# Kernel tuning notes

Hardware: AMD Instinct MI355X
Metric: run time of the kernel (lower is better)

## Reference

```python
import jax, jax.numpy as jnp
import numpy as np

N_EMBD = 384
HEAD_SIZE = 64
BLOCK_SIZE = 256

def setup_inputs() -> dict:
    key = jax.random.key(0)
    kx, kk, kq, kv = jax.random.split(key, 4)
    bound = 1.0 / np.sqrt(N_EMBD)  # torch nn.Linear default init
    return {
        "x": jax.random.normal(kx, (512, 256, N_EMBD), dtype=jnp.float32),
        "Wk": jax.random.uniform(kk, (N_EMBD, HEAD_SIZE), jnp.float32, -bound, bound),
        "Wq": jax.random.uniform(kq, (N_EMBD, HEAD_SIZE), jnp.float32, -bound, bound),
        "Wv": jax.random.uniform(kv, (N_EMBD, HEAD_SIZE), jnp.float32, -bound, bound),
    }

def reference(x, Wk, Wq, Wv):
    # x: [B, T, C]; single causal self-attention head (eval mode: dropout off)
    B, T, C = x.shape
    k = jnp.einsum('btc,ch->bth', x, Wk)   # [B, T, H]
    q = jnp.einsum('btc,ch->bth', x, Wq)
    v = jnp.einsum('btc,ch->bth', x, Wv)
    scale = 1.0 / jnp.sqrt(jnp.asarray(k.shape[-1], dtype=x.dtype))
    wei = jnp.einsum('bth,bsh->bts', q, k) * scale  # [B, T, T]
    causal = jnp.tril(jnp.ones((T, T), dtype=bool))
    wei = jnp.where(causal, wei, -jnp.inf)
    wei = jax.nn.softmax(wei, axis=-1)
    return jnp.einsum('bts,bsh->bth', wei, v)  # [B, T, H]
```

## Files before the change

kernel.cpp:

```cpp
#include <hip/hip_runtime.h>

#define T_DIM 256
#define C_DIM 384
#define H_DIM 64

typedef __attribute__((ext_vector_type(4))) float f32x4;
typedef __attribute__((ext_vector_type(8))) short bf16x8;
typedef unsigned short u16;

__device__ __forceinline__ u16 f2b(float f) {
  unsigned u = __float_as_uint(f);
  u = (u + 0x7FFFu + ((u >> 16) & 1u)) >> 16;
  return (u16)u;
}

__device__ __forceinline__ int sw64(int r, int c)  { return r * 64  + (c ^ ((r & 7) << 3)); }
__device__ __forceinline__ int sw256(int h, int t) { return h * 256 + (t ^ ((h & 7) << 3)); }
__device__ __forceinline__ int sw32(int r, int c)  { return r * 32  + (c ^ (((r >> 1) & 3) << 3)); }

__global__ __launch_bounds__(512, 2)
void head_fused(const float* __restrict__ x,
                const float* __restrict__ Wk,
                const float* __restrict__ Wq,
                const float* __restrict__ Wv,
                float* __restrict__ out)
{
  __shared__ u16 qs[T_DIM * H_DIM];
  __shared__ u16 ks[T_DIM * H_DIM];
  __shared__ u16 vT[H_DIM * T_DIM];
  __shared__ u16 un[16384];

  u16* xs  = un;
  u16* wsT = un + 8192;

  const int tid  = threadIdx.x;
  const int wv   = tid >> 6;
  const int lane = tid & 63;
  const int g    = lane >> 4;
  const int lr   = lane & 15;
  const int b    = blockIdx.x;

  const float* xb = x + (size_t)b * (T_DIM * C_DIM);

  int xr[4], xc[4];
#pragma unroll
  for (int it = 0; it < 4; ++it) {
    int idx = tid + it * 512;
    xr[it] = idx >> 3;
    xc[it] = (idx & 7) * 4;
  }
  int wrow[3], wcc[3];
  const float* wsrc[3];
#pragma unroll
  for (int it = 0; it < 3; ++it) {
    int idx = tid + it * 512;
    int q   = idx >> 5;
    int cc  = idx & 31;
    int seg = q >> 4;
    int hq  = q & 15;
    wrow[it] = seg * 64 + hq * 4;
    wcc[it]  = cc;
    wsrc[it] = ((seg == 0) ? Wq : (seg == 1) ? Wk : Wv) + hq * 4;
  }

  f32x4 acc[2][12];
#pragma unroll
  for (int mi = 0; mi < 2; ++mi)
#pragma unroll
    for (int nj = 0; nj < 12; ++nj)
      acc[mi][nj] = (f32x4){0.f, 0.f, 0.f, 0.f};

  f32x4 px[4], pwv[3];
#pragma unroll
  for (int it = 0; it < 4; ++it)
    px[it] = *reinterpret_cast<const f32x4*>(xb + xr[it] * C_DIM + xc[it]);
#pragma unroll
  for (int it = 0; it < 3; ++it)
    pwv[it] = *reinterpret_cast<const f32x4*>(wsrc[it] + wcc[it] * H_DIM);

  for (int kt = 0; kt < 12; ++kt) {
    __syncthreads();
#pragma unroll
    for (int it = 0; it < 4; ++it) {
      unsigned p0 = (unsigned)f2b(px[it][0]) | ((unsigned)f2b(px[it][1]) << 16);
      unsigned p1 = (unsigned)f2b(px[it][2]) | ((unsigned)f2b(px[it][3]) << 16);
      uint2 pv; pv.x = p0; pv.y = p1;
      *reinterpret_cast<uint2*>(&xs[sw32(xr[it], xc[it])]) = pv;
    }
#pragma unroll
    for (int it = 0; it < 3; ++it) {
      wsT[sw32(wrow[it] + 0, wcc[it])] = f2b(pwv[it][0]);
      wsT[sw32(wrow[it] + 1, wcc[it])] = f2b(pwv[it][1]);
      wsT[sw32(wrow[it] + 2, wcc[it])] = f2b(pwv[it][2]);
      wsT[sw32(wrow[it] + 3, wcc[it])] = f2b(pwv[it][3]);
    }
    if (kt < 11) {
      int kk = (kt + 1) * 32;
#pragma unroll
      for (int it = 0; it < 4; ++it)
        px[it] = *reinterpret_cast<const f32x4*>(xb + xr[it] * C_DIM + kk + xc[it]);
#pragma unroll
      for (int it = 0; it < 3; ++it)
        pwv[it] = *reinterpret_cast<const f32x4*>(wsrc[it] + (kk + wcc[it]) * H_DIM);
    }
    __syncthreads();

    bf16x8 afr[2];
#pragma unroll
    for (int mi = 0; mi < 2; ++mi)
      afr[mi] = *reinterpret_cast<const bf16x8*>(&xs[sw32(wv * 32 + mi * 16 + lr, g * 8)]);
#pragma unroll
    for (int nj = 0; nj < 12; ++nj) {
      bf16x8 bfr = *reinterpret_cast<const bf16x8*>(&wsT[sw32(nj * 16 + lr, g * 8)]);
#pragma unroll
      for (int mi = 0; mi < 2; ++mi)
        acc[mi][nj] = __builtin_amdgcn_mfma_f32_16x16x32_bf16(afr[mi], bfr, acc[mi][nj], 0, 0, 0);
    }
  }

#pragma unroll
  for (int mi = 0; mi < 2; ++mi)
#pragma unroll
    for (int nj = 0; nj < 12; ++nj)
#pragma unroll
      for (int e = 0; e < 4; ++e) {
        int r = wv * 32 + mi * 16 + g * 4 + e;
        int n = nj * 16 + lr;
        u16 val = f2b(acc[mi][nj][e]);
        if (n < 64)       qs[sw64(r, n)] = val;
        else if (n < 128) ks[sw64(r, n - 64)] = val;
        else              vT[sw256(n - 128, r)] = val;
      }
  __syncthreads();

  const int r0   = wv * 32;
  const int jmax = wv >> 1;
  u16* pw = un + wv * 2048;

  bf16x8 qf[2][2];
#pragma unroll
  for (int mi = 0; mi < 2; ++mi)
#pragma unroll
    for (int kb = 0; kb < 2; ++kb)
      qf[mi][kb] = *reinterpret_cast<const bf16x8*>(&qs[sw64(r0 + mi * 16 + lr, kb * 32 + g * 8)]);

  f32x4 o[2][4];
  float m_run[2][4], l_run[2][4];
#pragma unroll
  for (int mi = 0; mi < 2; ++mi) {
#pragma unroll
    for (int e = 0; e < 4; ++e) { m_run[mi][e] = -__builtin_inff(); l_run[mi][e] = 0.f; }
#pragma unroll
    for (int nh = 0; nh < 4; ++nh) o[mi][nh] = (f32x4){0.f, 0.f, 0.f, 0.f};
  }

  for (int j = 0; j <= jmax; ++j) {
    f32x4 s[2][4];
#pragma unroll
    for (int mi = 0; mi < 2; ++mi)
#pragma unroll
      for (int nj = 0; nj < 4; ++nj)
        s[mi][nj] = (f32x4){0.f, 0.f, 0.f, 0.f};
#pragma unroll
    for (int kb = 0; kb < 2; ++kb) {
#pragma unroll
      for (int nj = 0; nj < 4; ++nj) {
        bf16x8 kf = *reinterpret_cast<const bf16x8*>(&ks[sw64(j * 64 + nj * 16 + lr, kb * 32 + g * 8)]);
#pragma unroll
        for (int mi = 0; mi < 2; ++mi)
          s[mi][nj] = __builtin_amdgcn_mfma_f32_16x16x32_bf16(qf[mi][kb], kf, s[mi][nj], 0, 0, 0);
      }
    }
    float pm[2][4];
#pragma unroll
    for (int mi = 0; mi < 2; ++mi)
#pragma unroll
      for (int e = 0; e < 4; ++e) pm[mi][e] = -__builtin_inff();
#pragma unroll
    for (int mi = 0; mi < 2; ++mi)
#pragma unroll
      for (int nj = 0; nj < 4; ++nj)
#pragma unroll
        for (int e = 0; e < 4; ++e) {
          float v = s[mi][nj][e] * 0.125f;
          int r  = r0 + mi * 16 + g * 4 + e;
          int kv = j * 64 + nj * 16 + lr;
          v = (kv > r) ? -__builtin_inff() : v;
          s[mi][nj][e] = v;
          pm[mi][e] = fmaxf(pm[mi][e], v);
        }
#pragma unroll
    for (int off = 1; off < 16; off <<= 1)
#pragma unroll
      for (int mi = 0; mi < 2; ++mi)
#pragma unroll
        for (int e = 0; e < 4; ++e)
          pm[mi][e] = fmaxf(pm[mi][e], __shfl_xor(pm[mi][e], off));

    float rs[2][4];
#pragma unroll
    for (int mi = 0; mi < 2; ++mi)
#pragma unroll
      for (int e = 0; e < 4; ++e) {
        float mn = fmaxf(m_run[mi][e], pm[mi][e]);
        float alpha = __expf(m_run[mi][e] - mn);
        m_run[mi][e] = mn;
        l_run[mi][e] *= alpha;
        rs[mi][e] = 0.f;
#pragma unroll
        for (int nh = 0; nh < 4; ++nh) o[mi][nh][e] *= alpha;
      }
#pragma unroll
    for (int mi = 0; mi < 2; ++mi)
#pragma unroll
      for (int nj = 0; nj < 4; ++nj)
#pragma unroll
        for (int e = 0; e < 4; ++e) {
          float p = __expf(s[mi][nj][e] - m_run[mi][e]);
          s[mi][nj][e] = p;
          rs[mi][e] += p;
        }
#pragma unroll
    for (int off = 1; off < 16; off <<= 1)
#pragma unroll
      for (int mi = 0; mi < 2; ++mi)
#pragma unroll
        for (int e = 0; e < 4; ++e)
          rs[mi][e] += __shfl_xor(rs[mi][e], off);
#pragma unroll
    for (int mi = 0; mi < 2; ++mi)
#pragma unroll
      for (int e = 0; e < 4; ++e) l_run[mi][e] += rs[mi][e];

#pragma unroll
    for (int mi = 0; mi < 2; ++mi)
#pragma unroll
      for (int nj = 0; nj < 4; ++nj)
#pragma unroll
        for (int e = 0; e < 4; ++e) {
          int rr = mi * 16 + g * 4 + e;
          int cc = nj * 16 + lr;
          pw[sw64(rr, cc)] = f2b(s[mi][nj][e]);
        }
    asm volatile("s_waitcnt lgkmcnt(0)" ::: "memory");

#pragma unroll
    for (int kb = 0; kb < 2; ++kb) {
      bf16x8 pf[2];
#pragma unroll
      for (int mi = 0; mi < 2; ++mi)
        pf[mi] = *reinterpret_cast<const bf16x8*>(&pw[sw64(mi * 16 + lr, kb * 32 + g * 8)]);
#pragma unroll
      for (int nh = 0; nh < 4; ++nh) {
        bf16x8 vf = *reinterpret_cast<const bf16x8*>(&vT[sw256(nh * 16 + lr, j * 64 + kb * 32 + g * 8)]);
#pragma unroll
        for (int mi = 0; mi < 2; ++mi)
          o[mi][nh] = __builtin_amdgcn_mfma_f32_16x16x32_bf16(pf[mi], vf, o[mi][nh], 0, 0, 0);
      }
    }
  }

  float* ob = out + (size_t)b * (T_DIM * H_DIM);
  float linv[2][4];
#pragma unroll
  for (int mi = 0; mi < 2; ++mi)
#pragma unroll
    for (int e = 0; e < 4; ++e) linv[mi][e] = 1.f / l_run[mi][e];
#pragma unroll
  for (int mi = 0; mi < 2; ++mi)
#pragma unroll
    for (int nh = 0; nh < 4; ++nh)
#pragma unroll
      for (int e = 0; e < 4; ++e) {
        int r = r0 + mi * 16 + g * 4 + e;
        int h = nh * 16 + lr;
        ob[r * H_DIM + h] = o[mi][nh][e] * linv[mi][e];
      }
}

extern "C" void kernel_launch(void* const* d_in, const int* in_sizes, int n_in,
                              void* d_out, int out_size, void* d_ws, size_t ws_size,
                              hipStream_t stream) {
  const float* x  = (const float*)d_in[0];
  const float* Wk = (const float*)d_in[1];
  const float* Wq = (const float*)d_in[2];
  const float* Wv = (const float*)d_in[3];
  float* out = (float*)d_out;
  int B = in_sizes[0] / (T_DIM * C_DIM);
  head_fused<<<dim3(B), dim3(512), 0, stream>>>(x, Wk, Wq, Wv, out);
}
```

Before: 67.16 us.

## Shrink LDS footprint and compute transposed scores to keep P in registers

```diff
diff --git a/kernel.cpp b/kernel.cpp
--- a/kernel.cpp
+++ b/kernel.cpp
@@ -13,25 +13,28 @@
   u = (u + 0x7FFFu + ((u >> 16) & 1u)) >> 16;
   return (u16)u;
 }
+__device__ __forceinline__ unsigned pkbf(float a, float b) {
+  unsigned r;
+  asm("v_cvt_pk_bf16_f32 %0, %1, %2" : "=v"(r) : "v"(a), "v"(b));
+  return r;
+}
 
 __device__ __forceinline__ int sw64(int r, int c)  { return r * 64  + (c ^ ((r & 7) << 3)); }
 __device__ __forceinline__ int sw256(int h, int t) { return h * 256 + (t ^ ((h & 7) << 3)); }
 __device__ __forceinline__ int sw32(int r, int c)  { return r * 32  + (c ^ (((r >> 1) & 3) << 3)); }
 
-__global__ __launch_bounds__(512, 2)
+__global__ __launch_bounds__(512, 4)
 void head_fused(const float* __restrict__ x,
                 const float* __restrict__ Wk,
                 const float* __restrict__ Wq,
                 const float* __restrict__ Wv,
                 float* __restrict__ out)
 {
-  __shared__ u16 qs[T_DIM * H_DIM];
-  __shared__ u16 ks[T_DIM * H_DIM];
-  __shared__ u16 vT[H_DIM * T_DIM];
-  __shared__ u16 un[16384];
-
-  u16* xs  = un;
-  u16* wsT = un + 8192;
+  __shared__ u16 sh[32768];
+  u16* xs  = sh;
+  u16* wsT = sh + 8192;
+  u16* ks  = sh;
+  u16* vT  = sh + 16384;
 
   const int tid  = threadIdx.x;
   const int wv   = tid >> 6;
@@ -118,164 +121,161 @@
     }
   }
 
-#pragma unroll
-  for (int mi = 0; mi < 2; ++mi)
-#pragma unroll
-    for (int nj = 0; nj < 12; ++nj)
+  __syncthreads();
+
+  u16* slab = sh + wv * 2048;
+#pragma unroll
+  for (int mi = 0; mi < 2; ++mi)
+#pragma unroll
+    for (int nj = 0; nj < 4; ++nj)
+#pragma unroll
+      for (int e = 0; e < 4; ++e)
+        slab[sw64(mi * 16 + g * 4 + e, nj * 16 + lr)] = f2b(acc[mi][nj][e]);
+  asm volatile("s_waitcnt lgkmcnt(0)" ::: "memory");
+
+  bf16x8 qf[2][2];
+#pragma unroll
+  for (int mi = 0; mi < 2; ++mi)
+#pragma unroll
+    for (int kb = 0; kb < 2; ++kb)
+      qf[mi][kb] = *reinterpret_cast<const bf16x8*>(&slab[sw64(mi * 16 + lr, kb * 32 + g * 8)]);
+  __syncthreads();
+
+#pragma unroll
+  for (int mi = 0; mi < 2; ++mi)
+#pragma unroll
+    for (int nj = 4; nj < 12; ++nj)
 #pragma unroll
       for (int e = 0; e < 4; ++e) {
         int r = wv * 32 + mi * 16 + g * 4 + e;
         int n = nj * 16 + lr;
         u16 val = f2b(acc[mi][nj][e]);
-        if (n < 64)       qs[sw64(r, n)] = val;
-        else if (n < 128) ks[sw64(r, n - 64)] = val;
-        else              vT[sw256(n - 128, r)] = val;
+        if (n < 128) ks[sw64(r, n - 64)] = val;
+        else         vT[sw256(n - 128, r)] = val;
       }
   __syncthreads();
 
   const int r0   = wv * 32;
   const int jmax = wv >> 1;
-  u16* pw = un + wv * 2048;
-
-  bf16x8 qf[2][2];
-#pragma unroll
-  for (int mi = 0; mi < 2; ++mi)
-#pragma unroll
-    for (int kb = 0; kb < 2; ++kb)
-      qf[mi][kb] = *reinterpret_cast<const bf16x8*>(&qs[sw64(r0 + mi * 16 + lr, kb * 32 + g * 8)]);
 
   f32x4 o[2][4];
-  float m_run[2][4], l_run[2][4];
+  float m_run[2], l_run[2];
 #pragma unroll
   for (int mi = 0; mi < 2; ++mi) {
-#pragma unroll
-    for (int e = 0; e < 4; ++e) { m_run[mi][e] = -__builtin_inff(); l_run[mi][e] = 0.f; }
+    m_run[mi] = -__builtin_inff();
+    l_run[mi] = 0.f;
 #pragma unroll
     for (int nh = 0; nh < 4; ++nh) o[mi][nh] = (f32x4){0.f, 0.f, 0.f, 0.f};
   }
 
   for (int j = 0; j <= jmax; ++j) {
-    f32x4 s[2][4];
+    f32x4 sT[2][4];
 #pragma unroll
     for (int mi = 0; mi < 2; ++mi)
 #pragma unroll
-      for (int nj = 0; nj < 4; ++nj)
-        s[mi][nj] = (f32x4){0.f, 0.f, 0.f, 0.f};
+      for (int ni = 0; ni < 4; ++ni)
+        sT[mi][ni] = (f32x4){0.f, 0.f, 0.f, 0.f};
 #pragma unroll
     for (int kb = 0; kb < 2; ++kb) {
 #pragma unroll
-      for (int nj = 0; nj < 4; ++nj) {
-        bf16x8 kf = *reinterpret_cast<const bf16x8*>(&ks[sw64(j * 64 + nj * 16 + lr, kb * 32 + g * 8)]);
+      for (int ni = 0; ni < 4; ++ni) {
+        bf16x8 kf = *reinterpret_cast<const bf16x8*>(&ks[sw64(j * 64 + ni * 16 + lr, kb * 32 + g * 8)]);
 #pragma unroll
         for (int mi = 0; mi < 2; ++mi)
-          s[mi][nj] = __builtin_amdgcn_mfma_f32_16x16x32_bf16(qf[mi][kb], kf, s[mi][nj], 0, 0, 0);
-      }
-    }
-    float pm[2][4];
-#pragma unroll
-    for (int mi = 0; mi < 2; ++mi)
-#pragma unroll
-      for (int e = 0; e < 4; ++e) pm[mi][e] = -__builtin_inff();
-#pragma unroll
-    for (int mi = 0; mi < 2; ++mi)
-#pragma unroll
-      for (int nj = 0; nj < 4; ++nj)
+          sT[mi][ni] = __builtin_amdgcn_mfma_f32_16x16x32_bf16(kf, qf[mi][kb], sT[mi][ni], 0, 0, 0);
+      }
+    }
+
+#pragma unroll
+    for (int mi = 0; mi < 2; ++mi) {
+      const int q = r0 + mi * 16 + lr;
+      float pm = -__builtin_inff();
+#pragma unroll
+      for (int ni = 0; ni < 4; ++ni)
 #pragma unroll
         for (int e = 0; e < 4; ++e) {
-          float v = s[mi][nj][e] * 0.125f;
-          int r  = r0 + mi * 16 + g * 4 + e;
-          int kv = j * 64 + nj * 16 + lr;
-          v = (kv > r) ? -__builtin_inff() : v;
-          s[mi][nj][e] = v;
-          pm[mi][e] = fmaxf(pm[mi][e], v);
+          float v = sT[mi][ni][e] * 0.125f;
+          int kv = j * 64 + ni * 16 + g * 4 + e;
+          v = (kv > q) ? -__builtin_inff() : v;
+          sT[mi][ni][e] = v;
+          pm = fmaxf(pm, v);
         }
-#pragma unroll
-    for (int off = 1; off < 16; off <<= 1)
-#pragma unroll
-      for (int mi = 0; mi < 2; ++mi)
-#pragma unroll
-        for (int e = 0; e < 4; ++e)
-          pm[mi][e] = fmaxf(pm[mi][e], __shfl_xor(pm[mi][e], off));
-
-    float rs[2][4];
-#pragma unroll
-    for (int mi = 0; mi < 2; ++mi)
+      pm = fmaxf(pm, __shfl_xor(pm, 16));
+      pm = fmaxf(pm, __shfl_xor(pm, 32));
+
+      float mn = fmaxf(m_run[mi], pm);
+      float alpha = __expf(m_run[mi] - mn);
+      m_run[mi] = mn;
+      float rs = 0.f;
+#pragma unroll
+      for (int ni = 0; ni < 4; ++ni)
+#pragma unroll
+        for (int e = 0; e < 4; ++e) {
+          float p = __expf(sT[mi][ni][e] - mn);
+          sT[mi][ni][e] = p;
+          rs += p;
+        }
+      rs += __shfl_xor(rs, 16);
+      rs += __shfl_xor(rs, 32);
+      l_run[mi] = l_run[mi] * alpha + rs;
+
 #pragma unroll
       for (int e = 0; e < 4; ++e) {
-        float mn = fmaxf(m_run[mi][e], pm[mi][e]);
-        float alpha = __expf(m_run[mi][e] - mn);
-        m_run[mi][e] = mn;
-        l_run[mi][e] *= alpha;
-        rs[mi][e] = 0.f;
-#pragma unroll
-        for (int nh = 0; nh < 4; ++nh) o[mi][nh][e] *= alpha;
-      }
-#pragma unroll
-    for (int mi = 0; mi < 2; ++mi)
-#pragma unroll
-      for (int nj = 0; nj < 4; ++nj)
-#pragma unroll
-        for (int e = 0; e < 4; ++e) {
-          float p = __expf(s[mi][nj][e] - m_run[mi][e]);
-          s[mi][nj][e] = p;
-          rs[mi][e] += p;
+        float am = __shfl(alpha, g * 4 + e);
+#pragma unroll
+        for (int nh = 0; nh < 4; ++nh) o[mi][nh][e] *= am;
+      }
+    }
+
+    union PA { unsigned w[4]; bf16x8 v; };
+    PA pa[2][2];
+#pragma unroll
+    for (int mi = 0; mi < 2; ++mi) {
+      unsigned pk[4][2];
+#pragma unroll
+      for (int ni = 0; ni < 4; ++ni) {
+        pk[ni][0] = pkbf(sT[mi][ni][0], sT[mi][ni][1]);
+        pk[ni][1] = pkbf(sT[mi][ni][2], sT[mi][ni][3]);
+      }
+#pragma unroll
+      for (int kb = 0; kb < 2; ++kb)
+#pragma unroll
+        for (int w = 0; w < 4; ++w) {
+          int sl = ((2 * g + (w >> 1)) & 3) * 16 + lr;
+          unsigned lo = __shfl(pk[2 * kb + 0][w & 1], sl);
+          unsigned hi = __shfl(pk[2 * kb + 1][w & 1], sl);
+          pa[mi][kb].w[w] = (g >= 2) ? hi : lo;
         }
-#pragma unroll
-    for (int off = 1; off < 16; off <<= 1)
-#pragma unroll
-      for (int mi = 0; mi < 2; ++mi)
-#pragma unroll
-        for (int e = 0; e < 4; ++e)
-          rs[mi][e] += __shfl_xor(rs[mi][e], off);
-#pragma unroll
-    for (int mi = 0; mi < 2; ++mi)
-#pragma unroll
-      for (int e = 0; e < 4; ++e) l_run[mi][e] += rs[mi][e];
-
-#pragma unroll
-    for (int mi = 0; mi < 2; ++mi)
-#pragma unroll
-      for (int nj = 0; nj < 4; ++nj)
-#pragma unroll
-        for (int e = 0; e < 4; ++e) {
-          int rr = mi * 16 + g * 4 + e;
-          int cc = nj * 16 + lr;
-          pw[sw64(rr, cc)] = f2b(s[mi][nj][e]);
-        }
-    asm volatile("s_waitcnt lgkmcnt(0)" ::: "memory");
+    }
 
 #pragma unroll
     for (int kb = 0; kb < 2; ++kb) {
-      bf16x8 pf[2];
-#pragma unroll
-      for (int mi = 0; mi < 2; ++mi)
-        pf[mi] = *reinterpret_cast<const bf16x8*>(&pw[sw64(mi * 16 + lr, kb * 32 + g * 8)]);
 #pragma unroll
       for (int nh = 0; nh < 4; ++nh) {
         bf16x8 vf = *reinterpret_cast<const bf16x8*>(&vT[sw256(nh * 16 + lr, j * 64 + kb * 32 + g * 8)]);
 #pragma unroll
         for (int mi = 0; mi < 2; ++mi)
-          o[mi][nh] = __builtin_amdgcn_mfma_f32_16x16x32_bf16(pf[mi], vf, o[mi][nh], 0, 0, 0);
+          o[mi][nh] = __builtin_amdgcn_mfma_f32_16x16x32_bf16(pa[mi][kb].v, vf, o[mi][nh], 0, 0, 0);
       }
     }
   }
 
   float* ob = out + (size_t)b * (T_DIM * H_DIM);
-  float linv[2][4];
-#pragma unroll
-  for (int mi = 0; mi < 2; ++mi)
-#pragma unroll
-    for (int e = 0; e < 4; ++e) linv[mi][e] = 1.f / l_run[mi][e];
-#pragma unroll
-  for (int mi = 0; mi < 2; ++mi)
+#pragma unroll
+  for (int mi = 0; mi < 2; ++mi) {
+    float linv[4];
+#pragma unroll
+    for (int e = 0; e < 4; ++e)
+      linv[e] = 1.f / __shfl(l_run[mi], g * 4 + e);
 #pragma unroll
     for (int nh = 0; nh < 4; ++nh)
 #pragma unroll
       for (int e = 0; e < 4; ++e) {
         int r = r0 + mi * 16 + g * 4 + e;
         int h = nh * 16 + lr;
-        ob[r * H_DIM + h] = o[mi][nh][e] * linv[mi][e];
-      }
+        ob[r * H_DIM + h] = o[mi][nh][e] * linv[e];
+      }
+  }
 }
 
 extern "C" void kernel_launch(void* const* d_in, const int* in_sizes, int n_in,
```

Measured after the change: 210.9 us. 3.14x slower.
